# Performance work log

Hardware: AMD Instinct MI355X
Metric: run time of the kernel (lower is better)

The kernel has to match this reference:

```python
import jax, jax.numpy as jnp
import numpy as np

N_NODES = 50000
N_EDGES = 800000
N_FEAT = 128
DIM = 64
N_GRAPHS = 512


def setup_inputs() -> dict:
    key = jax.random.key(0)
    k1, k2, k3, k4, k5, k6 = jax.random.split(key, 6)
    x = jax.random.normal(k1, (N_NODES, N_FEAT), dtype=jnp.float32)
    edge_index = jax.random.randint(k2, (2, N_EDGES), 0, N_NODES, dtype=jnp.int64)
    batch = jnp.sort(jax.random.randint(k3, (N_NODES,), 0, N_GRAPHS, dtype=jnp.int64))
    W1 = jax.random.normal(k4, (N_FEAT, DIM), dtype=jnp.float32) * 0.05
    W2 = jax.random.normal(k5, (DIM, DIM), dtype=jnp.float32) * 0.05
    Wfc = jax.random.normal(k6, (DIM, 1), dtype=jnp.float32) * 0.05
    return {"x": x, "edge_index": edge_index, "batch": batch,
            "W1": W1, "W2": W2, "Wfc": Wfc}


def _gcn_conv(h, src, dst, W):
    # GCNConv(normalize=False, bias=False): linear transform then scatter-add
    # over edges: out[dst] += (h @ W)[src]
    h = jnp.einsum('nf,fd->nd', h, W)
    return jax.ops.segment_sum(h[src], dst, num_segments=N_NODES)


def reference(x, edge_index, batch, W1, W2, Wfc):
    src, dst = edge_index[0], edge_index[1]
    h = jax.nn.relu(_gcn_conv(x, src, dst, W1))          # [N, DIM]
    h = _gcn_conv(h, src, dst, W2)                        # [N, DIM]
    # global_mean_pool over graph ids
    counts = jax.ops.segment_sum(jnp.ones((N_NODES,), h.dtype), batch,
                                 num_segments=N_GRAPHS)   # [G]
    pooled = jax.ops.segment_sum(h, batch, num_segments=N_GRAPHS)
    pooled = pooled / jnp.maximum(counts, 1.0)[:, None]   # [G, DIM]
    return jax.nn.sigmoid(pooled @ Wfc)                   # [G, 1]
```

## Files before the change

kernel.cpp:

```cpp
#include <hip/hip_runtime.h>
#include <cmath>

#define N_NODES 50000
#define N_EDGES 800000
#define N_FEAT 128
#define DIM 64
#define N_GRAPHS 512
#define GGRID ((N_NODES + 63) / 64)
#define NBKT GGRID
#define BH_BLK 128
#define EPB (N_EDGES / BH_BLK)
#define NCNT (NBKT * BH_BLK)
#define P2_NBLK ((NCNT + 511) / 512)
#define BKT_CAP 2048

typedef short short8 __attribute__((ext_vector_type(8)));
typedef float floatx4 __attribute__((ext_vector_type(4)));

__device__ __forceinline__ unsigned short f2bf(float f) {
  union { float f; unsigned int u; } v; v.f = f;
  return (unsigned short)((v.u + 0x7FFFu + ((v.u >> 16) & 1u)) >> 16);
}
__device__ __forceinline__ float bf2f(unsigned short u) {
  union { unsigned int u; float f; } v; v.u = (unsigned int)u << 16;
  return v.f;
}

__global__ __launch_bounds__(256) void bhist_w2fc(const int* __restrict__ dst,
                                                  int* __restrict__ cnt,
                                                  const float* __restrict__ W2,
                                                  const float* __restrict__ Wfc,
                                                  float* __restrict__ w2fc,
                                                  const float* __restrict__ W1,
                                                  unsigned short* __restrict__ w1sh,
                                                  unsigned short* __restrict__ w1sl) {
  if (blockIdx.x == BH_BLK) {
    int k = threadIdx.x;
    if (k < 64) {
      float s = 0.f;
#pragma unroll 8
      for (int j = 0; j < 64; j++) s += W2[k * 64 + j] * Wfc[j];
      w2fc[k] = s;
    }
    return;
  }
  if (blockIdx.x == BH_BLK + 1) {
    int tid = threadIdx.x;
#pragma unroll
    for (int i = 0; i < 32; i++) {
      int idx = i * 256 + tid;
      int kk = idx & 127, c = idx >> 7;
      float f = W1[kk * 64 + c];
      unsigned short h = f2bf(f);
      unsigned short l = f2bf(f - bf2f(h));
      int didx = c * 128 + (kk ^ ((c & 15) << 3));
      w1sh[didx] = h;
      w1sl[didx] = l;
    }
    return;
  }
  __shared__ int lh[NBKT];
  const int tid = threadIdx.x, k = blockIdx.x;
  for (int i = tid; i < NBKT; i += 256) lh[i] = 0;
  __syncthreads();
  const int base = k * EPB;
  for (int j = tid; j < EPB; j += 256)
    atomicAdd(&lh[dst[base + j] >> 6], 1);
  __syncthreads();
  for (int i = tid; i < NBKT; i += 256) cnt[i * BH_BLK + k] = lh[i];
}

__global__ __launch_bounds__(256) void f_psum(const int* __restrict__ cnt,
                                              int* __restrict__ partials) {
  __shared__ int ws[4];
  const int tid = threadIdx.x;
  const int2* cnt2 = (const int2*)cnt;
  int idx = blockIdx.x * 256 + tid;
  int v = 0;
  if (idx * 2 < NCNT) { int2 c = cnt2[idx]; v = c.x + c.y; }
#pragma unroll
  for (int off = 32; off; off >>= 1) v += __shfl_down(v, off, 64);
  int lane = tid & 63, w = tid >> 6;
  if (lane == 0) ws[w] = v;
  __syncthreads();
  if (tid == 0) partials[blockIdx.x] = ws[0] + ws[1] + ws[2] + ws[3];
}

__global__ __launch_bounds__(256) void f_sblocks(int* __restrict__ cnt,
                                                 const int* __restrict__ partials,
                                                 int* __restrict__ bucket_ptr) {
  __shared__ int buf[256];
  __shared__ int pbuf[256];
  const int tid = threadIdx.x;
  int2* cnt2 = (int2*)cnt;
  const int idx = blockIdx.x * 256 + tid;
  int2 c = make_int2(0, 0);
  if (idx * 2 < NCNT) c = cnt2[idx];
  int s = c.x + c.y;
  buf[tid] = s;
  pbuf[tid] = (tid < P2_NBLK) ? partials[tid] : 0;
  __syncthreads();
  for (int off = 1; off < 256; off <<= 1) {
    int t1 = (tid >= off) ? buf[tid - off] : 0;
    int t2 = (tid >= off) ? pbuf[tid - off] : 0;
    __syncthreads();
    buf[tid] += t1;
    pbuf[tid] += t2;
    __syncthreads();
  }
  const int thr_excl = buf[tid] - s;
  const int base = (blockIdx.x > 0) ? pbuf[blockIdx.x - 1] : 0;
  if (idx * 2 < NCNT) {
    int e0 = base + thr_excl;
    cnt2[idx] = make_int2(e0, e0 + c.x);
    int p = idx * 2;
    if ((p & (BH_BLK - 1)) == 0) bucket_ptr[p >> 7] = e0;
    if (p + 1 == NCNT - 1) bucket_ptr[NBKT] = e0 + c.x + c.y;
  }
}

__device__ __forceinline__ void gemm1_mfma(const float* __restrict__ x,
                                           const unsigned short* __restrict__ w1sh,
                                           const unsigned short* __restrict__ w1sl,
                                           unsigned short* __restrict__ h1,
                                           int row0, int tid,
                                           unsigned short* sXh, unsigned short* sXl,
                                           unsigned short* sWh, unsigned short* sWl) {
  const int4* wh4 = (const int4*)w1sh;
  const int4* wl4 = (const int4*)w1sl;
  int4* sWh4 = (int4*)sWh;
  int4* sWl4 = (int4*)sWl;
#pragma unroll
  for (int i = 0; i < 4; i++) {
    sWh4[i * 256 + tid] = wh4[i * 256 + tid];
    sWl4[i * 256 + tid] = wl4[i * 256 + tid];
  }
#pragma unroll
  for (int i = 0; i < 8; i++) {
    int fid = i * 256 + tid;
    int r = fid >> 5;
    int c4 = (fid & 31) << 2;
    int gr = row0 + r;
    float4 v = make_float4(0.f, 0.f, 0.f, 0.f);
    if (gr < N_NODES) v = *(const float4*)&x[(size_t)gr * N_FEAT + c4];
    ushort4 h, l;
    h.x = f2bf(v.x); l.x = f2bf(v.x - bf2f(h.x));
    h.y = f2bf(v.y); l.y = f2bf(v.y - bf2f(h.y));
    h.z = f2bf(v.z); l.z = f2bf(v.z - bf2f(h.z));
    h.w = f2bf(v.w); l.w = f2bf(v.w - bf2f(h.w));
    int idx = r * 128 + (c4 ^ ((r & 15) << 3));
    *(ushort4*)&sXh[idx] = h;
    *(ushort4*)&sXl[idx] = l;
  }
  __syncthreads();

  const int lane = tid & 63, w = tid >> 6;
  const int g = lane >> 4, c15 = lane & 15;
  const int ra = (w << 4) + c15;
  const int akey = c15 << 3;
  floatx4 acc[4];
#pragma unroll
  for (int i = 0; i < 4; i++) acc[i] = (floatx4){0.f, 0.f, 0.f, 0.f};

#pragma unroll
  for (int kb = 0; kb < 128; kb += 32) {
    const int ka = kb + g * 8;
    short8 ah = *(const short8*)&sXh[ra * 128 + (ka ^ akey)];
    short8 al = *(const short8*)&sXl[ra * 128 + (ka ^ akey)];
#pragma unroll
    for (int ct = 0; ct < 4; ct++) {
      const int cb = ct * 16 + c15;
      const int bi = cb * 128 + (ka ^ akey);
      short8 bh = *(const short8*)&sWh[bi];
      short8 bl = *(const short8*)&sWl[bi];
      acc[ct] = __builtin_amdgcn_mfma_f32_16x16x32_bf16(ah, bh, acc[ct], 0, 0, 0);
      acc[ct] = __builtin_amdgcn_mfma_f32_16x16x32_bf16(ah, bl, acc[ct], 0, 0, 0);
      acc[ct] = __builtin_amdgcn_mfma_f32_16x16x32_bf16(al, bh, acc[ct], 0, 0, 0);
    }
  }

#pragma unroll
  for (int ct = 0; ct < 4; ct++) {
#pragma unroll
    for (int r = 0; r < 4; r++) {
      int gr = row0 + (w << 4) + (g << 2) + r;
      if (gr < N_NODES) h1[(size_t)gr * 64 + ct * 16 + c15] = f2bf(acc[ct][r]);
    }
  }
}

__global__ __launch_bounds__(256) void gemm1_bscatter(
    const float* __restrict__ x,
    const unsigned short* __restrict__ w1sh,
    const unsigned short* __restrict__ w1sl,
    unsigned short* __restrict__ h1, const int* __restrict__ src,
    const int* __restrict__ dst, const int* __restrict__ cnt,
    unsigned int* __restrict__ ebuf) {
  __shared__ __align__(16) unsigned short sXh[64 * 128];
  __shared__ __align__(16) unsigned short sXl[64 * 128];
  __shared__ __align__(16) unsigned short sWh[64 * 128];
  __shared__ __align__(16) unsigned short sWl[64 * 128];
  const int tid = threadIdx.x;
  if (blockIdx.x < GGRID) {
    gemm1_mfma(x, w1sh, w1sl, h1, blockIdx.x * 64, tid, sXh, sXl, sWh, sWl);
  } else {
    int* loff = (int*)sXh;
    const int k = blockIdx.x - GGRID;
    for (int i = tid; i < NBKT; i += 256) loff[i] = cnt[i * BH_BLK + k];
    __syncthreads();
    const int base = k * EPB;
    for (int j = tid; j < EPB; j += 256) {
      int e = base + j;
      int d = dst[e];
      int pos = atomicAdd(&loff[d >> 6], 1);
      ebuf[pos] = ((unsigned int)src[e] << 6) | (unsigned int)(d & 63);
    }
  }
}

__global__ __launch_bounds__(1024, 8) void gather_z_fused(
    const unsigned short* __restrict__ h1,
    const unsigned int* __restrict__ ebuf,
    const int* __restrict__ bucket_ptr,
    const float* __restrict__ w2fc,
    float* __restrict__ z) {
  __shared__ int colL[BKT_CAP];
  __shared__ int lstart[64];
  __shared__ int lcur[64];
  __shared__ float sw[64];
  const int tid = threadIdx.x;
  const int b = blockIdx.x;
  const int p0 = bucket_ptr[b];
  int cnt = bucket_ptr[b + 1] - p0;
  if (cnt > BKT_CAP) cnt = BKT_CAP;

  if (tid < 64) { lstart[tid] = 0; sw[tid] = w2fc[tid]; }
  __syncthreads();
  for (int i = tid; i < cnt; i += 1024)
    atomicAdd(&lstart[ebuf[p0 + i] & 63], 1);
  __syncthreads();
  if (tid < 64) {
    int v = lstart[tid], s = v;
#pragma unroll
    for (int off = 1; off < 64; off <<= 1) {
      int t = __shfl_up(s, off, 64);
      if (tid >= off) s += t;
    }
    lstart[tid] = s - v;
    lcur[tid] = s - v;
  }
  __syncthreads();
  for (int i = tid; i < cnt; i += 1024) {
    unsigned int u = ebuf[p0 + i];
    int pos = atomicAdd(&lcur[u & 63], 1);
    colL[pos] = (int)(u >> 6);
  }
  __syncthreads();

  const int lane = tid & 63, w = tid >> 6;
  const int eo = lane >> 4, qfo = (lane & 15) << 2;
#pragma unroll
  for (int ni = 0; ni < 4; ni++) {
    const int r = ni * 16 + w;
    const int i1 = lcur[r];
    int i = lstart[r];
    float4 acc = make_float4(0.f, 0.f, 0.f, 0.f);
    for (; i + 16 <= i1; i += 16) {
      int s0 = colL[i + eo];
      int s1 = colL[i + 4 + eo];
      int s2 = colL[i + 8 + eo];
      int s3 = colL[i + 12 + eo];
      ushort4 u0 = *(const ushort4*)&h1[(size_t)s0 * 64 + qfo];
      ushort4 u1 = *(const ushort4*)&h1[(size_t)s1 * 64 + qfo];
      ushort4 u2 = *(const ushort4*)&h1[(size_t)s2 * 64 + qfo];
      ushort4 u3 = *(const ushort4*)&h1[(size_t)s3 * 64 + qfo];
      acc.x += (bf2f(u0.x) + bf2f(u1.x)) + (bf2f(u2.x) + bf2f(u3.x));
      acc.y += (bf2f(u0.y) + bf2f(u1.y)) + (bf2f(u2.y) + bf2f(u3.y));
      acc.z += (bf2f(u0.z) + bf2f(u1.z)) + (bf2f(u2.z) + bf2f(u3.z));
      acc.w += (bf2f(u0.w) + bf2f(u1.w)) + (bf2f(u2.w) + bf2f(u3.w));
    }
    for (; i + 4 <= i1; i += 4) {
      int s = colL[i + eo];
      ushort4 u = *(const ushort4*)&h1[(size_t)s * 64 + qfo];
      acc.x += bf2f(u.x); acc.y += bf2f(u.y);
      acc.z += bf2f(u.z); acc.w += bf2f(u.w);
    }
    if (eo < i1 - i) {
      int s = colL[i + eo];
      ushort4 u = *(const ushort4*)&h1[(size_t)s * 64 + qfo];
      acc.x += bf2f(u.x); acc.y += bf2f(u.y);
      acc.z += bf2f(u.z); acc.w += bf2f(u.w);
    }
#pragma unroll
    for (int m = 16; m <= 32; m <<= 1) {
      acc.x += __shfl_xor(acc.x, m, 64);
      acc.y += __shfl_xor(acc.y, m, 64);
      acc.z += __shfl_xor(acc.z, m, 64);
      acc.w += __shfl_xor(acc.w, m, 64);
    }
    float p = fmaxf(acc.x, 0.f) * sw[qfo] + fmaxf(acc.y, 0.f) * sw[qfo + 1] +
              fmaxf(acc.z, 0.f) * sw[qfo + 2] + fmaxf(acc.w, 0.f) * sw[qfo + 3];
#pragma unroll
    for (int m = 1; m <= 8; m <<= 1) p += __shfl_xor(p, m, 64);
    int node = b * 64 + r;
    if (lane == 0 && node < N_NODES) z[node] = p;
  }
}

__global__ __launch_bounds__(256) void graph_pool(const float* __restrict__ z,
                                                  const unsigned int* __restrict__ ebuf,
                                                  const int* __restrict__ bucket_ptr,
                                                  const int* __restrict__ batch,
                                                  float* __restrict__ out) {
  __shared__ float sacc[4];
  int g = blockIdx.x;
  int tid = threadIdx.x, lane = tid & 63, w = tid >> 6;

  int lo = 0, hi = N_NODES;
  while (lo < hi) { int mid = (lo + hi) >> 1; if (batch[mid] < g) lo = mid + 1; else hi = mid; }
  const int start = lo;
  hi = N_NODES;
  while (lo < hi) { int mid = (lo + hi) >> 1; if (batch[mid] < g + 1) lo = mid + 1; else hi = mid; }
  const int end = lo;

  float s = 0.f;
  if (end > start) {
    const int b0 = start >> 6, b1 = ((end - 1) >> 6) + 1;
    for (int b = b0; b < b1; b++) {
      const int q0 = bucket_ptr[b], q1 = bucket_ptr[b + 1];
      const int base = b << 6;
      for (int i = q0 + tid; i < q1; i += 256) {
        unsigned int u = ebuf[i];
        int d = base + (int)(u & 63);
        if (d >= start && d < end) s += z[u >> 6];
      }
    }
  }
#pragma unroll
  for (int off = 32; off; off >>= 1) s += __shfl_down(s, off, 64);
  if (lane == 0) sacc[w] = s;
  __syncthreads();
  if (tid == 0) {
    float v = sacc[0] + sacc[1] + sacc[2] + sacc[3];
    v /= fmaxf((float)(end - start), 1.f);
    out[g] = 1.f / (1.f + expf(-v));
  }
}

extern "C" void kernel_launch(void* const* d_in, const int* in_sizes, int n_in,
                              void* d_out, int out_size, void* d_ws, size_t ws_size,
                              hipStream_t stream) {
  const float* x     = (const float*)d_in[0];
  const int*   ei    = (const int*)d_in[1];
  const int*   batch = (const int*)d_in[2];
  const float* W1    = (const float*)d_in[3];
  const float* W2    = (const float*)d_in[4];
  const float* Wfc   = (const float*)d_in[5];
  float*       out   = (float*)d_out;

  const int* src = ei;
  const int* dst = ei + N_EDGES;

  char* ws = (char*)d_ws;
  unsigned short* h1 = (unsigned short*)(ws);
  unsigned short* w1sh = (unsigned short*)(ws + (size_t)N_NODES * DIM * 2);
  unsigned short* w1sl = w1sh + N_FEAT * DIM;
  float* z    = (float*)(w1sl + N_FEAT * DIM);
  float* w2fc = z + N_NODES;
  int*   cnt  = (int*)(w2fc + 64);
  int*   partials = cnt + NCNT;
  unsigned int* ebuf = (unsigned int*)(partials + P2_NBLK);
  int*   bucket_ptr  = (int*)(ebuf + N_EDGES);

  bhist_w2fc<<<BH_BLK + 2, 256, 0, stream>>>(dst, cnt, W2, Wfc, w2fc,
                                             W1, w1sh, w1sl);
  f_psum<<<P2_NBLK, 256, 0, stream>>>(cnt, partials);
  f_sblocks<<<P2_NBLK, 256, 0, stream>>>(cnt, partials, bucket_ptr);

  gemm1_bscatter<<<GGRID + BH_BLK, 256, 0, stream>>>(x, w1sh, w1sl, h1, src,
                                                     dst, cnt, ebuf);

  gather_z_fused<<<NBKT, 1024, 0, stream>>>(h1, ebuf, bucket_ptr, w2fc, z);

  graph_pool<<<N_GRAPHS, 256, 0, stream>>>(z, ebuf, bucket_ptr, batch, out);
}
```

Baseline: 151.8 us.

## Drop LDS staging in GEMM1, load X and W1 fragments directly from global

The first GEMM no longer stages X and the hi/lo bf16 W1 split through 64 KB of shared memory. Each lane now loads its own X row fragment from global memory, splits it to bf16 hi/lo in registers, and reads W1 fragments straight from global/L2 in an unswizzled layout. This frees LDS, which should raise occupancy and remove a block-wide barrier. The bucket-scatter blocks are also moved to the front of the grid so they start first. In exchange there are more redundant global and L2 reads of W1 across waves, and the X loads are less coalesced.

Measured after the change: 153.9 us. About the same (+1.4%).

```diff
diff --git a/kernel.cpp b/kernel.cpp
--- a/kernel.cpp
+++ b/kernel.cpp
@@ -53,9 +53,8 @@
       float f = W1[kk * 64 + c];
       unsigned short h = f2bf(f);
       unsigned short l = f2bf(f - bf2f(h));
-      int didx = c * 128 + (kk ^ ((c & 15) << 3));
-      w1sh[didx] = h;
-      w1sl[didx] = l;
+      w1sh[idx] = h;
+      w1sl[idx] = l;
     }
     return;
   }
@@ -123,41 +122,12 @@
                                            const unsigned short* __restrict__ w1sh,
                                            const unsigned short* __restrict__ w1sl,
                                            unsigned short* __restrict__ h1,
-                                           int row0, int tid,
-                                           unsigned short* sXh, unsigned short* sXl,
-                                           unsigned short* sWh, unsigned short* sWl) {
-  const int4* wh4 = (const int4*)w1sh;
-  const int4* wl4 = (const int4*)w1sl;
-  int4* sWh4 = (int4*)sWh;
-  int4* sWl4 = (int4*)sWl;
-#pragma unroll
-  for (int i = 0; i < 4; i++) {
-    sWh4[i * 256 + tid] = wh4[i * 256 + tid];
-    sWl4[i * 256 + tid] = wl4[i * 256 + tid];
-  }
-#pragma unroll
-  for (int i = 0; i < 8; i++) {
-    int fid = i * 256 + tid;
-    int r = fid >> 5;
-    int c4 = (fid & 31) << 2;
-    int gr = row0 + r;
-    float4 v = make_float4(0.f, 0.f, 0.f, 0.f);
-    if (gr < N_NODES) v = *(const float4*)&x[(size_t)gr * N_FEAT + c4];
-    ushort4 h, l;
-    h.x = f2bf(v.x); l.x = f2bf(v.x - bf2f(h.x));
-    h.y = f2bf(v.y); l.y = f2bf(v.y - bf2f(h.y));
-    h.z = f2bf(v.z); l.z = f2bf(v.z - bf2f(h.z));
-    h.w = f2bf(v.w); l.w = f2bf(v.w - bf2f(h.w));
-    int idx = r * 128 + (c4 ^ ((r & 15) << 3));
-    *(ushort4*)&sXh[idx] = h;
-    *(ushort4*)&sXl[idx] = l;
-  }
-  __syncthreads();
-
+                                           int row0, int tid) {
   const int lane = tid & 63, w = tid >> 6;
   const int g = lane >> 4, c15 = lane & 15;
-  const int ra = (w << 4) + c15;
-  const int akey = c15 << 3;
+  const int ra = row0 + (w << 4) + c15;
+  const bool va = ra < N_NODES;
+  const float* xr = &x[(size_t)(va ? ra : 0) * N_FEAT];
   floatx4 acc[4];
 #pragma unroll
   for (int i = 0; i < 4; i++) acc[i] = (floatx4){0.f, 0.f, 0.f, 0.f};
@@ -165,14 +135,24 @@
 #pragma unroll
   for (int kb = 0; kb < 128; kb += 32) {
     const int ka = kb + g * 8;
-    short8 ah = *(const short8*)&sXh[ra * 128 + (ka ^ akey)];
-    short8 al = *(const short8*)&sXl[ra * 128 + (ka ^ akey)];
+    float4 v0 = make_float4(0.f, 0.f, 0.f, 0.f), v1 = v0;
+    if (va) {
+      v0 = *(const float4*)&xr[ka];
+      v1 = *(const float4*)&xr[ka + 4];
+    }
+    const float fv[8] = {v0.x, v0.y, v0.z, v0.w, v1.x, v1.y, v1.z, v1.w};
+    short8 ah, al;
+#pragma unroll
+    for (int j = 0; j < 8; j++) {
+      unsigned short h = f2bf(fv[j]);
+      ah[j] = (short)h;
+      al[j] = (short)f2bf(fv[j] - bf2f(h));
+    }
 #pragma unroll
     for (int ct = 0; ct < 4; ct++) {
       const int cb = ct * 16 + c15;
-      const int bi = cb * 128 + (ka ^ akey);
-      short8 bh = *(const short8*)&sWh[bi];
-      short8 bl = *(const short8*)&sWl[bi];
+      short8 bh = *(const short8*)&w1sh[cb * 128 + ka];
+      short8 bl = *(const short8*)&w1sl[cb * 128 + ka];
       acc[ct] = __builtin_amdgcn_mfma_f32_16x16x32_bf16(ah, bh, acc[ct], 0, 0, 0);
       acc[ct] = __builtin_amdgcn_mfma_f32_16x16x32_bf16(ah, bl, acc[ct], 0, 0, 0);
       acc[ct] = __builtin_amdgcn_mfma_f32_16x16x32_bf16(al, bh, acc[ct], 0, 0, 0);
@@ -196,16 +176,12 @@
     unsigned short* __restrict__ h1, const int* __restrict__ src,
     const int* __restrict__ dst, const int* __restrict__ cnt,
     unsigned int* __restrict__ ebuf) {
-  __shared__ __align__(16) unsigned short sXh[64 * 128];
-  __shared__ __align__(16) unsigned short sXl[64 * 128];
-  __shared__ __align__(16) unsigned short sWh[64 * 128];
-  __shared__ __align__(16) unsigned short sWl[64 * 128];
+  __shared__ int loff[NBKT];
   const int tid = threadIdx.x;
-  if (blockIdx.x < GGRID) {
-    gemm1_mfma(x, w1sh, w1sl, h1, blockIdx.x * 64, tid, sXh, sXl, sWh, sWl);
+  if (blockIdx.x >= BH_BLK) {
+    gemm1_mfma(x, w1sh, w1sl, h1, (blockIdx.x - BH_BLK) * 64, tid);
   } else {
-    int* loff = (int*)sXh;
-    const int k = blockIdx.x - GGRID;
+    const int k = blockIdx.x;
     for (int i = tid; i < NBKT; i += 256) loff[i] = cnt[i * BH_BLK + k];
     __syncthreads();
     const int base = k * EPB;
```
